# Kernel optimization log

Measured on AMD Instinct MI355X. Metric: run time of the kernel, lower is better.

Reference implementation:

```python
import jax, jax.numpy as jnp
import numpy as np

N_NODES = 50000
N_EDGES = 800000
IN_DIM = 2
HID = 256
OUT = 16
MLP_H = 256
N_MID = 10  # middle GCN layers (256->256); total 12 layers
EPS = 1e-5


def _bn(x, g, b):
    # BatchNorm1d forward with batch statistics (training-mode math, deterministic)
    m = jnp.mean(x, axis=0)
    v = jnp.var(x, axis=0)
    return (x - m) * jax.lax.rsqrt(v + EPS) * g + b


def _conv(h, W, b, row, col, ew):
    # CutGCNConv: linear transform then edge-weighted scatter-add (source->target)
    h = h @ W + b                      # [N, out]
    msg = ew[:, None] * h[row]         # gather + scale, [E, out]
    return jax.ops.segment_sum(msg, col, num_segments=N_NODES)


def setup_inputs() -> dict:
    key = jax.random.key(0)
    ks = iter(jax.random.split(key, 32))
    d = {}
    d["x"] = jax.random.normal(next(ks), (N_NODES, IN_DIM), dtype=jnp.float32)
    d["edge_index"] = jax.random.randint(next(ks), (2, N_EDGES), 0, N_NODES, dtype=jnp.int32)
    d["edge_weight"] = jax.random.uniform(next(ks), (N_EDGES,), dtype=jnp.float32)
    # GCN params
    d["W0"] = jax.random.normal(next(ks), (IN_DIM, HID), dtype=jnp.float32) / np.sqrt(IN_DIM)
    d["b0"] = jnp.zeros((HID,), jnp.float32)
    d["Wm"] = jax.random.normal(next(ks), (N_MID, HID, HID), dtype=jnp.float32) / np.sqrt(HID)
    d["bm"] = jnp.zeros((N_MID, HID), jnp.float32)
    d["Wl"] = jax.random.normal(next(ks), (HID, OUT), dtype=jnp.float32) / np.sqrt(HID)
    d["bl"] = jnp.zeros((OUT,), jnp.float32)
    # BatchNorms: one before each GCN layer + one after the stack
    d["bn0_g"] = jnp.ones((IN_DIM,), jnp.float32); d["bn0_b"] = jnp.zeros((IN_DIM,), jnp.float32)
    d["bnm_g"] = jnp.ones((N_MID + 1, HID), jnp.float32); d["bnm_b"] = jnp.zeros((N_MID + 1, HID), jnp.float32)
    d["bno_g"] = jnp.ones((OUT,), jnp.float32); d["bno_b"] = jnp.zeros((OUT,), jnp.float32)
    # edge MLP params
    d["mW1"] = jax.random.normal(next(ks), (2 * OUT, MLP_H), dtype=jnp.float32) / np.sqrt(2 * OUT)
    d["mb1"] = jnp.zeros((MLP_H,), jnp.float32)
    d["mbn_g"] = jnp.ones((MLP_H,), jnp.float32); d["mbn_b"] = jnp.zeros((MLP_H,), jnp.float32)
    d["mW2"] = jax.random.normal(next(ks), (MLP_H, 1), dtype=jnp.float32) / np.sqrt(MLP_H)
    d["mb2"] = jnp.zeros((1,), jnp.float32)
    return d


def reference(x, edge_index, edge_weight, W0, b0, Wm, bm, Wl, bl,
              bn0_g, bn0_b, bnm_g, bnm_b, bno_g, bno_b,
              mW1, mb1, mbn_g, mbn_b, mW2, mb2):
    row, col = edge_index[0], edge_index[1]
    # GCN stack (dropout is identity in eval; ReLU after each conv)
    h = jax.nn.relu(_conv(_bn(x, bn0_g, bn0_b), W0, b0, row, col, edge_weight))
    for i in range(N_MID):
        h = jax.nn.relu(_conv(_bn(h, bnm_g[i], bnm_b[i]), Wm[i], bm[i], row, col, edge_weight))
    h = jax.nn.relu(_conv(_bn(h, bnm_g[N_MID], bnm_b[N_MID]), Wl, bl, row, col, edge_weight))
    h = _bn(h, bno_g, bno_b)  # final BatchNorm on gnn_out_dims

    def mlp(e):  # e: [E, 2*OUT]
        z = jax.nn.relu(_bn(e @ mW1 + mb1, mbn_g, mbn_b))
        return (z @ mW2 + mb2)[:, 0]

    hr, hc = h[row], h[col]
    p1 = mlp(jnp.concatenate([hr, hc], axis=1))
    # roll(shifts=16, dims=1) on a 32-wide tensor swaps the halves
    p2 = mlp(jnp.concatenate([hc, hr], axis=1))
    return jax.nn.sigmoid(0.5 * (p1 + p2))
```

## Files before the change

### kernel.cpp

```cpp
#include <hip/hip_runtime.h>
#include <hip/hip_bf16.h>
#include <hip/hip_fp16.h>
#include <math.h>

#define NNODES 50000
#define NEDGES 800000

#define OFF_CW       0ull
#define OFF_DOUT     401408ull
#define OFF_STATS2   602112ull
#define OFF_SP8      606208ull
#define OFF_MOM      966656ull
#define ZERO_END     1017856ull
#define OFF_ST       1017856ull
#define OFF_ABW      1019904ull
#define OFF_WIN      1026048ull
#define OFF_OFFSETS  1226752ull
#define OFF_SROW     1427456ull
#define OFF_SEW      4627456ull
#define OFF_RANK     7827456ull
#define OFF_WT       11027456ull
#define OFF_WP       12338176ull
#define OFF_BUFQ     12371968ull
#define OFF_BUFP     37971968ull
#define ALI_TMP16    0ull
#define ALI_HRAW     3276800ull
#define ALI_Z        6553600ull
#define ALI_AGGZ     8388608ull

typedef __attribute__((ext_vector_type(8))) _Float16 f16x8;
typedef __attribute__((ext_vector_type(4))) float f32x4;

union H4 { ushort4 u; __half h[4]; };
union US8 { uint4 u; __half h[8]; };
union HU { ushort u; __half h; };

static __device__ inline ushort f2h(float f) {
    HU cv; cv.h = __float2half(f); return cv.u;
}
static __device__ inline float h2f(ushort u) {
    HU cv; cv.u = u; return __half2float(cv.h);
}


__global__ void hist_kernel(const int* __restrict__ ei, const float* __restrict__ ew,
                            unsigned long long* __restrict__ cw, int* __restrict__ dout,
                            int* __restrict__ rank, int E) {
    for (int i = blockIdx.x * blockDim.x + threadIdx.x; i < E; i += gridDim.x * blockDim.x) {
        int r = ei[i];
        int c = ei[E + i];
        unsigned long long pack = (1ull << 40) |
            (unsigned long long)__float2uint_rn(ew[i] * 1048576.f);
        unsigned long long old = atomicAdd(&cw[c], pack);
        rank[i] = (int)(old >> 40);
        atomicAdd(&dout[r], 1);
    }
}

__global__ void scan_kernel(const unsigned long long* __restrict__ cw,
                            int* __restrict__ offsets, float* __restrict__ w_in, int N) {
    __shared__ int wsum[16];
    __shared__ int carry_s;
    int tid = threadIdx.x;
    int lane = tid & 63, w = tid >> 6;
    if (tid == 0) carry_s = 0;
    __syncthreads();
    for (int base = 0; base < N; base += 1024) {
        int v = 0;
        if (base + tid < N) {
            unsigned long long cv = cw[base + tid];
            v = (int)(cv >> 40);
            w_in[base + tid] = (float)(cv & 0xFFFFFFFFFFull) * (1.f / 1048576.f);
        }
        int x = v;
#pragma unroll
        for (int off = 1; off < 64; off <<= 1) {
            int y = __shfl_up(x, off);
            if (lane >= off) x += y;
        }
        if (lane == 63) wsum[w] = x;
        __syncthreads();
        if (w == 0 && lane < 16) {
            int s = wsum[lane];
#pragma unroll
            for (int off = 1; off < 16; off <<= 1) {
                int y = __shfl_up(s, off);
                if (lane >= off) s += y;
            }
            wsum[lane] = s;
        }
        __syncthreads();
        int wbase = (w > 0) ? wsum[w - 1] : 0;
        int incl = carry_s + wbase + x;
        if (base + tid < N) offsets[base + tid] = incl - v;
        __syncthreads();
        if (tid == 0) carry_s += wsum[15];
        __syncthreads();
    }
    if (tid == 0) offsets[N] = carry_s;
}

__global__ void scatter_kernel(const int* __restrict__ ei, const float* __restrict__ ew,
                               const int* __restrict__ offsets, const int* __restrict__ rank,
                               int* __restrict__ srow, float* __restrict__ sew, int E) {
    for (int i = blockIdx.x * blockDim.x + threadIdx.x; i < E; i += gridDim.x * blockDim.x) {
        int c = ei[E + i];
        int p = offsets[c] + rank[i];
        srow[p] = ei[i];
        sew[p] = ew[i];
    }
}


__global__ __launch_bounds__(256) void wconv(const float* __restrict__ Wm,
                                             ushort* __restrict__ Wt) {
    __shared__ float tile[32][33];
    int b = blockIdx.x;
    int layer = b >> 6, t = b & 63;
    int tk = (t >> 3) << 5, tn = (t & 7) << 5;
    int tid = threadIdx.x;
    int r = tid >> 5, c = tid & 31;
    const float* W = Wm + layer * 65536;
#pragma unroll
    for (int i = 0; i < 4; i++) tile[r + i * 8][c] = W[(tk + r + i * 8) * 256 + tn + c];
    __syncthreads();
#pragma unroll
    for (int i = 0; i < 4; i++) {
        int n = tn + r + i * 8, k = tk + c;
        Wt[layer * 65536 + n * 256 + k] = f2h(tile[c][r + i * 8]);
    }
}

__global__ void wprep(const float* __restrict__ mW1, ushort* __restrict__ Wp) {
    int tid = threadIdx.x;
    for (int n = tid; n < 512; n += 256) {
        for (int k = 0; k < 32; k++) {
            float v;
            if (n < 256) v = mW1[k * 256 + n];
            else {
                int n2 = n - 256;
                v = (k < 16) ? mW1[(16 + k) * 256 + n2] : mW1[(k - 16) * 256 + n2];
            }
            Wp[n * 32 + k] = f2h(v);
        }
    }
}


__global__ __launch_bounds__(256) void colstats_wr(const float* __restrict__ h,
                                                   float* __restrict__ sums, int C, int M) {
    int gtid = blockIdx.x * blockDim.x + threadIdx.x;
    int lane = threadIdx.x & 63;
    int c = gtid % C;
    int r = gtid / C;
    int stride = (gridDim.x * blockDim.x) / C;
    float s = 0.f, q = 0.f;
    for (; r < M; r += stride) {
        float v = h[r * C + c];
        s += v; q += v * v;
    }
    for (int m = 32; m >= C; m >>= 1) {
        s += __shfl_xor(s, m);
        q += __shfl_xor(q, m);
    }
    if (lane < C) {
        atomicAdd(&sums[c], s);
        atomicAdd(&sums[C + c], q);
    }
}

__global__ void bn_finalize(const float* __restrict__ sums, const float* __restrict__ g,
                            const float* __restrict__ b, float* __restrict__ st, int C, int M) {
    int c = threadIdx.x;
    if (c >= C) return;
    float mean = sums[c] / (float)M;
    float var  = sums[C + c] / (float)M - mean * mean;
    float sc = g[c] * rsqrtf(var + 1e-5f);
    st[c] = sc;
    st[C + c] = b[c] - mean * sc;
}

__global__ void bn_finalize16(const float* __restrict__ sp, const float* __restrict__ g,
                              const float* __restrict__ b, float* __restrict__ st, int M) {
    int c = threadIdx.x;
    float s = 0.f, q = 0.f;
#pragma unroll
    for (int p = 0; p < 16; p++) { s += sp[p * 512 + c]; q += sp[p * 512 + 256 + c]; }
    float mean = s / (float)M;
    float var  = q / (float)M - mean * mean;
    float sc = g[c] * rsqrtf(var + 1e-5f);
    st[c] = sc;
    st[256 + c] = b[c] - mean * sc;
}


__global__ __launch_bounds__(256) void gemm_mfma(const __half* __restrict__ H,
                                                 const ushort* __restrict__ Wt,
                                                 const float* __restrict__ bias,
                                                 const float* __restrict__ sp,
                                                 const float* __restrict__ g,
                                                 const float* __restrict__ b,
                                                 __half* __restrict__ out, int M) {
    __shared__ __attribute__((aligned(16))) ushort Ah[128][40];
    __shared__ __attribute__((aligned(16))) ushort Bh[128][40];
    __shared__ __attribute__((aligned(16))) float st_s[512];
    int tid = threadIdx.x;
    int wid = tid >> 6, lane = tid & 63;
    int m0 = blockIdx.x * 128;
    int n0 = blockIdx.y * 128;
    const ushort* Hu = (const ushort*)H;

    {
        float s = 0.f, q = 0.f;
#pragma unroll
        for (int p = 0; p < 16; p++) { s += sp[p * 512 + tid]; q += sp[p * 512 + 256 + tid]; }
        float invM = 1.f / (float)M;
        float mean = s * invM;
        float var  = q * invM - mean * mean;
        float sc = g[tid] * rsqrtf(var + 1e-5f);
        st_s[tid] = sc;
        st_s[256 + tid] = b[tid] - mean * sc;
    }
    __syncthreads();

    f32x4 acc[2][8];
#pragma unroll
    for (int m = 0; m < 2; m++)
#pragma unroll
        for (int n = 0; n < 8; n++) acc[m][n] = (f32x4){0.f, 0.f, 0.f, 0.f};

    int sr = tid >> 3;
    int kq = (tid & 7) << 2;
    int fr = lane & 15;
    int qo = (lane >> 4) << 3;
    int mrow = wid << 5;

    for (int k0 = 0; k0 < 256; k0 += 32) {
#pragma unroll
        for (int t = 0; t < 4; t++) {
            int r = sr + t * 32;
            int gr = m0 + r; if (gr >= M) gr = M - 1;
            H4 h4; h4.u = *(const ushort4*)(Hu + gr * 256 + k0 + kq);
            float4 s4 = *(const float4*)(st_s + k0 + kq);
            float4 t4 = *(const float4*)(st_s + 256 + k0 + kq);
            ushort4 vh;
            vh.x = f2h(__half2float(h4.h[0]) * s4.x + t4.x);
            vh.y = f2h(__half2float(h4.h[1]) * s4.y + t4.y);
            vh.z = f2h(__half2float(h4.h[2]) * s4.z + t4.z);
            vh.w = f2h(__half2float(h4.h[3]) * s4.w + t4.w);
            *(ushort4*)&Ah[r][kq] = vh;
            ushort4 bh = *(const ushort4*)(Wt + (n0 + r) * 256 + k0 + kq);
            *(ushort4*)&Bh[r][kq] = bh;
        }
        __syncthreads();

        f16x8 a0 = *(const f16x8*)&Ah[mrow + fr][qo];
        f16x8 a1 = *(const f16x8*)&Ah[mrow + 16 + fr][qo];
#pragma unroll
        for (int nt = 0; nt < 8; nt++) {
            f16x8 bb = *(const f16x8*)&Bh[nt * 16 + fr][qo];
            acc[0][nt] = __builtin_amdgcn_mfma_f32_16x16x32_f16(a0, bb, acc[0][nt], 0, 0, 0);
            acc[1][nt] = __builtin_amdgcn_mfma_f32_16x16x32_f16(a1, bb, acc[1][nt], 0, 0, 0);
        }
        __syncthreads();
    }

#pragma unroll
    for (int mt = 0; mt < 2; mt++) {
        int gmb = m0 + mrow + mt * 16 + ((lane >> 4) << 2);
#pragma unroll
        for (int nt = 0; nt < 8; nt++) {
            int gn = n0 + nt * 16 + fr;
            float bv = bias[gn];
#pragma unroll
            for (int j = 0; j < 4; j++) {
                int gm = gmb + j;
                if (gm < M) out[gm * 256 + gn] = __float2half(acc[mt][nt][j] + bv);
            }
        }
    }
}


__global__ __launch_bounds__(256) void spmm_f16w(const __half* __restrict__ T,
                                                 const int* __restrict__ srow,
                                                 const float* __restrict__ sew,
                                                 const int* __restrict__ off,
                                                 __half* __restrict__ outp,
                                                 float* __restrict__ sp, int N) {
    __shared__ float red[4][512];
    int tid = threadIdx.x;
    int wid = tid >> 6, lane = tid & 63;
    int hh = lane >> 5;
    int li = lane & 31;
    int colb = li << 3;
    const ushort* Tu = (const ushort*)T;
    ushort* Ou = (ushort*)outp;
    float cs[8] = {0, 0, 0, 0, 0, 0, 0, 0}, cq[8] = {0, 0, 0, 0, 0, 0, 0, 0};
    int gw = blockIdx.x * 4 + wid, nw = gridDim.x * 4;
    for (int n = gw; n < N; n += nw) {
        int e0 = off[n], e1 = off[n + 1];
        float acc[8] = {0, 0, 0, 0, 0, 0, 0, 0};
        int e = e0;
        for (; e + 7 < e1; e += 8) {
            int rr[4]; float wv[4]; US8 v[4];
#pragma unroll
            for (int i = 0; i < 4; i++) { rr[i] = srow[e + 2 * i + hh]; wv[i] = sew[e + 2 * i + hh]; }
#pragma unroll
            for (int i = 0; i < 4; i++) v[i].u = *(const uint4*)(Tu + rr[i] * 256 + colb);
#pragma unroll
            for (int i = 0; i < 4; i++)
#pragma unroll
                for (int j = 0; j < 8; j++) acc[j] += wv[i] * __half2float(v[i].h[j]);
        }
        for (; e < e1; e += 2) {
            if (e + hh < e1) {
                int r = srow[e + hh]; float w = sew[e + hh];
                US8 v; v.u = *(const uint4*)(Tu + r * 256 + colb);
#pragma unroll
                for (int j = 0; j < 8; j++) acc[j] += w * __half2float(v.h[j]);
            }
        }
        US8 o;
#pragma unroll
        for (int j = 0; j < 8; j++) {
            float other = __shfl(acc[j], lane ^ 32, 64);
            float s = fmaxf(acc[j] + other, 0.f);
            o.h[j] = __float2half(s);
            if (hh == 0) { cs[j] += s; cq[j] += s * s; }
        }
        if (hh == 0) *(uint4*)(Ou + n * 256 + colb) = o.u;
    }
    if (hh == 0) {
#pragma unroll
        for (int j = 0; j < 8; j++) {
            red[wid][colb + j] = cs[j];
            red[wid][256 + colb + j] = cq[j];
        }
    }
    __syncthreads();
    float* dst = sp + (blockIdx.x & 15) * 512;
    for (int i = tid; i < 512; i += 256)
        atomicAdd(&dst[i], red[0][i] + red[1][i] + red[2][i] + red[3][i]);
}

__global__ __launch_bounds__(256) void spmm_small(const float* __restrict__ T,
                                                  const int* __restrict__ srow,
                                                  const float* __restrict__ sew,
                                                  const int* __restrict__ off,
                                                  float* __restrict__ out,
                                                  int C, int N, int relu) {
    int npb = blockDim.x / C;
    int local = threadIdx.x / C;
    int c = threadIdx.x % C;
    int n = blockIdx.x * npb + local;
    if (n >= N) return;
    int e0 = off[n], e1 = off[n + 1];
    float acc = 0.f;
    for (int e = e0; e < e1; ++e) acc += sew[e] * T[srow[e] * C + c];
    if (relu) acc = fmaxf(acc, 0.f);
    out[n * C + c] = acc;
}


__global__ __launch_bounds__(256) void layer0_fin(const float* __restrict__ agg2,
                                                  const float* __restrict__ w_in,
                                                  const float* __restrict__ st,
                                                  const float* __restrict__ W0,
                                                  const float* __restrict__ b0,
                                                  __half* __restrict__ h,
                                                  float* __restrict__ sp, int N) {
    int j = threadIdx.x;
    float w0j = W0[j], w1j = W0[256 + j], b0j = b0[j];
    float s0 = st[0], s1 = st[1], t0 = st[2], t1 = st[3];
    float cs = 0.f, cq = 0.f;
    for (int n = blockIdx.x; n < N; n += gridDim.x) {
        float wi = w_in[n];
        float a0 = agg2[n * 2 + 0] * s0 + wi * t0;
        float a1 = agg2[n * 2 + 1] * s1 + wi * t1;
        float v = fmaxf(a0 * w0j + a1 * w1j + wi * b0j, 0.f);
        h[n * 256 + j] = __float2half(v);
        cs += v; cq += v * v;
    }
    float* dst = sp + (blockIdx.x & 15) * 512;
    atomicAdd(&dst[j], cs);
    atomicAdd(&dst[256 + j], cq);
}


__global__ __launch_bounds__(256) void gemm16(const __half* __restrict__ H,
                                              const float* __restrict__ Wl,
                                              const float* __restrict__ bl,
                                              const float* __restrict__ st,
                                              float* __restrict__ out, int M) {
    __shared__ float Hs[16][256];
    __shared__ float Ws[256][16];
    int tid = threadIdx.x;
    int n0 = blockIdx.x << 4;
    const ushort* Hu = (const ushort*)H;
    for (int i = tid; i < 4096; i += 256) Ws[i >> 4][i & 15] = Wl[i];
    for (int i = tid; i < 4096; i += 256) {
        int r = i >> 8, k = i & 255;
        int n = n0 + r;
        float hv = 0.f;
        if (n < M) hv = h2f(Hu[n * 256 + k]) * st[k] + st[256 + k];
        Hs[r][k] = hv;
    }
    __syncthreads();
    int r = tid >> 4, j = tid & 15;
    float acc = bl[j];
    for (int k = 0; k < 256; k++) acc += Hs[r][k] * Ws[k][j];
    if (n0 + r < M) out[(n0 + r) * 16 + j] = acc;
}


__global__ void zprep(const float* __restrict__ hraw, const float* __restrict__ st,
                      ushort* __restrict__ Z, int NE) {
    int i = blockIdx.x * blockDim.x + threadIdx.x;
    if (i >= NE) return;
    int c = i & 15;
    Z[i] = f2h(hraw[i] * st[c] + st[16 + c]);
}


__global__ __launch_bounds__(256) void aggz_spmm(const ushort* __restrict__ Z,
                                                 const int* __restrict__ srow,
                                                 const int* __restrict__ off,
                                                 float* __restrict__ aggz, int N) {
    int local = threadIdx.x >> 4;
    int c = threadIdx.x & 15;
    int n = blockIdx.x * 16 + local;
    if (n >= N) return;
    int e0 = off[n], e1 = off[n + 1];
    float acc = 0.f;
    for (int e = e0; e < e1; ++e) acc += h2f(Z[srow[e] * 16 + c]);
    aggz[n * 16 + c] = acc;
}


__global__ __launch_bounds__(256) void zmom(const ushort* __restrict__ Z,
                                            const float* __restrict__ aggz,
                                            const int* __restrict__ dout,
                                            const unsigned long long* __restrict__ cw,
                                            float* __restrict__ MOM, int N) {
    __shared__ float zs[128][17];
    __shared__ float az[128][17];
    __shared__ float dw[128][2];
    int tid = threadIdx.x;
    int i = tid >> 4, j = tid & 15;
    float p = 0.f, r = 0.f, m = 0.f, sdo = 0.f, sdi = 0.f;
    for (int base = blockIdx.x * 128; base < N; base += gridDim.x * 128) {
        int cnt = N - base; if (cnt > 128) cnt = 128;
        for (int t = tid; t < 2048; t += 256) {
            int n = t >> 4, c = t & 15;
            if (n < cnt) {
                zs[n][c] = h2f(Z[(base + n) * 16 + c]);
                az[n][c] = aggz[(base + n) * 16 + c];
            } else { zs[n][c] = 0.f; az[n][c] = 0.f; }
        }
        for (int t = tid; t < 128; t += 256) {
            if (t < cnt) {
                dw[t][0] = (float)dout[base + t];
                dw[t][1] = (float)(int)(cw[base + t] >> 40);
            } else { dw[t][0] = 0.f; dw[t][1] = 0.f; }
        }
        __syncthreads();
        for (int n = 0; n < 128; n++) {
            float zi = zs[n][i], zj = zs[n][j];
            float d0 = dw[n][0], d1 = dw[n][1];
            float zz = zi * zj;
            p += d0 * zz;
            r += d1 * zz;
            m += az[n][i] * zj;
            if (i == 0) { sdo += d0 * zj; sdi += d1 * zj; }
        }
        __syncthreads();
    }
    float* dst = MOM + (blockIdx.x & 15) * 800;
    atomicAdd(&dst[tid], p);
    atomicAdd(&dst[256 + tid], r);
    atomicAdd(&dst[512 + tid], m);
    if (i == 0) { atomicAdd(&dst[768 + j], sdo); atomicAdd(&dst[784 + j], sdi); }
}


__global__ __launch_bounds__(256) void mlp_ab(const float* __restrict__ MOM,
                                              const float* __restrict__ mW1,
                                              const float* __restrict__ g,
                                              const float* __restrict__ b,
                                              const float* __restrict__ mW2,
                                              float* __restrict__ abw, int E) {
    __shared__ float P[256], R[256], Mm[256], Sdo[16], Sdi[16];
    int tid = threadIdx.x;
    float sp = 0.f, sr = 0.f, sm = 0.f;
#pragma unroll
    for (int q = 0; q < 16; q++) {
        sp += MOM[q * 800 + tid];
        sr += MOM[q * 800 + 256 + tid];
        sm += MOM[q * 800 + 512 + tid];
    }
    P[tid] = sp; R[tid] = sr; Mm[tid] = sm;
    if (tid < 16) {
        float a = 0.f, c = 0.f;
#pragma unroll
        for (int q = 0; q < 16; q++) { a += MOM[q * 800 + 768 + tid]; c += MOM[q * 800 + 784 + tid]; }
        Sdo[tid] = a; Sdi[tid] = c;
    }
    __syncthreads();
    int j = tid;
    float A[16], B[16];
#pragma unroll
    for (int k = 0; k < 16; k++) { A[k] = mW1[k * 256 + j]; B[k] = mW1[(16 + k) * 256 + j]; }
    float apa = 0.f, brb = 0.f, amb = 0.f, bpb = 0.f, ara = 0.f, bma = 0.f;
    float aso = 0.f, bso = 0.f, asi = 0.f, bsi = 0.f;
    for (int i2 = 0; i2 < 16; i2++) {
        float Ai = A[i2], Bi = B[i2];
        aso += Ai * Sdo[i2]; bso += Bi * Sdo[i2];
        asi += Ai * Sdi[i2]; bsi += Bi * Sdi[i2];
#pragma unroll
        for (int k = 0; k < 16; k++) {
            float Pik = P[i2 * 16 + k], Rik = R[i2 * 16 + k], Mik = Mm[i2 * 16 + k];
            apa += Ai * Pik * A[k]; brb += Bi * Rik * B[k]; amb += Ai * Mik * B[k];
            bpb += Bi * Pik * B[k]; ara += Ai * Rik * A[k]; bma += Bi * Mik * A[k];
        }
    }
    float invE = 1.f / (float)E;
    float mu1 = (aso + bsi) * invE;
    float mu2 = (bso + asi) * invE;
    float e21 = (apa + brb + 2.f * amb) * invE;
    float e22 = (bpb + ara + 2.f * bma) * invE;
    float v1 = e21 - mu1 * mu1;
    float v2 = e22 - mu2 * mu2;
    float a1 = g[j] * rsqrtf(v1 + 1e-5f);
    float a2 = g[j] * rsqrtf(v2 + 1e-5f);
    abw[j] = a1;                 abw[256 + j] = a2;
    abw[512 + j] = b[j] - mu1 * a1; abw[768 + j] = b[j] - mu2 * a2;
    abw[1024 + j] = mW2[j];      abw[1280 + j] = mW2[j];
}


__global__ __launch_bounds__(256) void edge_mfma(const ushort* __restrict__ Z,
                                                 const int* __restrict__ ei,
                                                 const ushort* __restrict__ Wp,
                                                 const float* __restrict__ abw,
                                                 const float* __restrict__ mb2,
                                                 float* __restrict__ out, int E) {
    __shared__ __attribute__((aligned(16))) ushort As[256][40];
    __shared__ __attribute__((aligned(16))) ushort Bs[512][40];
    int tid = threadIdx.x;
    int wid = tid >> 6, lane = tid & 63;
    int fr = lane & 15, qo = (lane >> 4) << 3;

    for (int i = tid * 4; i < 512 * 32; i += 1024) {
        int n = i >> 5, k = i & 31;
        *(ushort4*)&Bs[n][k] = *(const ushort4*)(Wp + i);
    }
    int e0 = blockIdx.x * 256;
    {
        int e = e0 + tid;
        int r = 0, c = 0;
        if (e < E) { r = ei[e]; c = ei[E + e]; }
        uint4 z0 = *(const uint4*)(Z + r * 16);
        uint4 z1 = *(const uint4*)(Z + r * 16 + 8);
        uint4 z2 = *(const uint4*)(Z + c * 16);
        uint4 z3 = *(const uint4*)(Z + c * 16 + 8);
        *(uint4*)&As[tid][0]  = z0; *(uint4*)&As[tid][8]  = z1;
        *(uint4*)&As[tid][16] = z2; *(uint4*)&As[tid][24] = z3;
    }
    __syncthreads();

    f16x8 a[4];
#pragma unroll
    for (int mt = 0; mt < 4; mt++) a[mt] = *(const f16x8*)&As[(wid * 4 + mt) * 16 + fr][qo];
    float pacc[4][4];
#pragma unroll
    for (int mt = 0; mt < 4; mt++)
#pragma unroll
        for (int j = 0; j < 4; j++) pacc[mt][j] = 0.f;
    float mb2v = mb2[0];

    for (int n = 0; n < 32; n++) {
        f16x8 bfr = *(const f16x8*)&Bs[n * 16 + fr][qo];
        int col = n * 16 + fr;
        float av = abw[col], bv = abw[512 + col], wv = abw[1024 + col];
#pragma unroll
        for (int mt = 0; mt < 4; mt++) {
            f32x4 c0 = {0.f, 0.f, 0.f, 0.f};
            c0 = __builtin_amdgcn_mfma_f32_16x16x32_f16(a[mt], bfr, c0, 0, 0, 0);
#pragma unroll
            for (int j = 0; j < 4; j++)
                pacc[mt][j] += fmaxf(c0[j] * av + bv, 0.f) * wv;
        }
    }

#pragma unroll
    for (int mt = 0; mt < 4; mt++)
#pragma unroll
        for (int j = 0; j < 4; j++) {
            float p = pacc[mt][j];
            p += __shfl_xor(p, 1);
            p += __shfl_xor(p, 2);
            p += __shfl_xor(p, 4);
            p += __shfl_xor(p, 8);
            if (fr == 0) {
                int row = (wid * 4 + mt) * 16 + ((lane >> 4) << 2) + j;
                int e = e0 + row;
                if (e < E) out[e] = 1.f / (1.f + expf(-(0.5f * p + mb2v)));
            }
        }
}


extern "C" void kernel_launch(void* const* d_in, const int* in_sizes, int n_in,
                              void* d_out, int out_size, void* d_ws, size_t ws_size,
                              hipStream_t stream) {
    const float* x     = (const float*)d_in[0];
    const int*   ei    = (const int*)d_in[1];
    const float* ew    = (const float*)d_in[2];
    const float* W0    = (const float*)d_in[3];
    const float* b0    = (const float*)d_in[4];
    const float* Wm    = (const float*)d_in[5];
    const float* bm    = (const float*)d_in[6];
    const float* Wl    = (const float*)d_in[7];
    const float* bl    = (const float*)d_in[8];
    const float* bn0_g = (const float*)d_in[9];
    const float* bn0_b = (const float*)d_in[10];
    const float* bnm_g = (const float*)d_in[11];
    const float* bnm_b = (const float*)d_in[12];
    const float* bno_g = (const float*)d_in[13];
    const float* bno_b = (const float*)d_in[14];
    const float* mW1   = (const float*)d_in[15];
    const float* mbn_g = (const float*)d_in[17];
    const float* mbn_b = (const float*)d_in[18];
    const float* mW2   = (const float*)d_in[19];
    const float* mb2   = (const float*)d_in[20];
    float* outp = (float*)d_out;

    char* ws = (char*)d_ws;
    unsigned long long* cw = (unsigned long long*)(ws + OFF_CW);
    int*    dout    = (int*)(ws + OFF_DOUT);
    float*  stats2  = (float*)(ws + OFF_STATS2);
    float*  sp8     = (float*)(ws + OFF_SP8);
    float*  MOM     = (float*)(ws + OFF_MOM);
    float*  st      = (float*)(ws + OFF_ST);
    float*  abw     = (float*)(ws + OFF_ABW);
    float*  w_in    = (float*)(ws + OFF_WIN);
    int*    offsets = (int*)(ws + OFF_OFFSETS);
    int*    srow    = (int*)(ws + OFF_SROW);
    float*  sew     = (float*)(ws + OFF_SEW);
    int*    rank    = (int*)(ws + OFF_RANK);
    ushort* Wt      = (ushort*)(ws + OFF_WT);
    ushort* Wp      = (ushort*)(ws + OFF_WP);
    __half* bufQ    = (__half*)(ws + OFF_BUFQ);
    __half* bufP    = (__half*)(ws + OFF_BUFP);
    float*  agg2    = (float*)(ws + OFF_BUFQ + ALI_TMP16);
    float*  tmp16   = (float*)(ws + OFF_BUFQ + ALI_TMP16);
    float*  hraw    = (float*)(ws + OFF_BUFQ + ALI_HRAW);
    ushort* Z       = (ushort*)(ws + OFF_BUFQ + ALI_Z);
    float*  aggz    = (float*)(ws + OFF_BUFQ + ALI_AGGZ);

    const int N = NNODES, E = NEDGES;

    hipMemsetAsync(ws, 0, ZERO_END, stream);

    hist_kernel<<<1024, 256, 0, stream>>>(ei, ew, cw, dout, rank, E);
    wconv<<<640, 256, 0, stream>>>(Wm, Wt);
    wprep<<<1, 256, 0, stream>>>(mW1, Wp);
    scan_kernel<<<1, 1024, 0, stream>>>(cw, offsets, w_in, N);
    scatter_kernel<<<1024, 256, 0, stream>>>(ei, ew, offsets, rank, srow, sew, E);

    colstats_wr<<<64, 256, 0, stream>>>(x, stats2 + 0 * 512, 2, N);
    bn_finalize<<<1, 256, 0, stream>>>(stats2 + 0 * 512, bn0_g, bn0_b, st, 2, N);
    spmm_small<<<(N + 127) / 128, 256, 0, stream>>>(x, srow, sew, offsets, agg2, 2, N, 0);
    layer0_fin<<<512, 256, 0, stream>>>(agg2, w_in, st, W0, b0, bufP, sp8 + 0 * 8192, N);

    for (int i = 0; i < 10; i++) {
        gemm_mfma<<<dim3((N + 127) / 128, 2), 256, 0, stream>>>(
            bufP, Wt + i * 65536, bm + i * 256,
            sp8 + i * 8192, bnm_g + i * 256, bnm_b + i * 256, bufQ, N);
        spmm_f16w<<<2048, 256, 0, stream>>>(bufQ, srow, sew, offsets, bufP,
                                            sp8 + (i + 1) * 8192, N);
    }

    bn_finalize16<<<1, 256, 0, stream>>>(sp8 + 10 * 8192, bnm_g + 10 * 256,
                                         bnm_b + 10 * 256, st, N);
    gemm16<<<(N + 15) / 16, 256, 0, stream>>>(bufP, Wl, bl, st, tmp16, N);
    spmm_small<<<(N + 15) / 16, 256, 0, stream>>>(tmp16, srow, sew, offsets, hraw, 16, N, 1);

    colstats_wr<<<64, 256, 0, stream>>>(hraw, stats2 + 1 * 512, 16, N);
    bn_finalize<<<1, 256, 0, stream>>>(stats2 + 1 * 512, bno_g, bno_b, st, 16, N);
    zprep<<<(N * 16 + 255) / 256, 256, 0, stream>>>(hraw, st, Z, N * 16);

    aggz_spmm<<<(N + 15) / 16, 256, 0, stream>>>(Z, srow, offsets, aggz, N);
    zmom<<<256, 256, 0, stream>>>(Z, aggz, dout, cw, MOM, N);
    mlp_ab<<<1, 256, 0, stream>>>(MOM, mW1, mbn_g, mbn_b, mW2, abw, E);

    edge_mfma<<<(E + 255) / 256, 256, 0, stream>>>(Z, ei, Wp, abw, mb2, outp, E);
}
```

Measured before the change: 1.544 ms.

## Fold BatchNorm into weights, pack CSR edges, rewrite edge MLP via abs identity

Folds each middle layer's BatchNorm scale and shift into a per-layer copy of the fp16 weights and bias, computed by a small bnw kernel. The GEMM A-tile load then becomes a plain copy instead of a per-element normalize. Row index and edge weight are packed into one int2 array, so each SpMM does one gather instead of two. The edge MLP folds the BN scale into Wp2 and rewrites relu(x) as (x+|x|)/2, so the linear half becomes a per-node dot product (gprep) and the kernel accumulates only |c+b|. This drops the shared-memory B staging, but the weights are no longer normalized in fp32 first, which may change rounding.

```diff
diff --git a/kernel.cpp b/kernel.cpp
--- a/kernel.cpp
+++ b/kernel.cpp
@@ -16,11 +16,12 @@
 #define OFF_ABW      1019904ull
 #define OFF_WIN      1026048ull
 #define OFF_OFFSETS  1226752ull
-#define OFF_SROW     1427456ull
-#define OFF_SEW      4627456ull
+#define OFF_SE       1427456ull
 #define OFF_RANK     7827456ull
+#define ALI_WT2      0ull
+#define ALI_BIAS2    131072ull
+#define ALI_G        132096ull
 #define OFF_WT       11027456ull
-#define OFF_WP       12338176ull
 #define OFF_BUFQ     12371968ull
 #define OFF_BUFP     37971968ull
 #define ALI_TMP16    0ull
@@ -102,12 +103,11 @@
 
 __global__ void scatter_kernel(const int* __restrict__ ei, const float* __restrict__ ew,
                                const int* __restrict__ offsets, const int* __restrict__ rank,
-                               int* __restrict__ srow, float* __restrict__ sew, int E) {
+                               int2* __restrict__ se, int E) {
     for (int i = blockIdx.x * blockDim.x + threadIdx.x; i < E; i += gridDim.x * blockDim.x) {
         int c = ei[E + i];
         int p = offsets[c] + rank[i];
-        srow[p] = ei[i];
-        sew[p] = ew[i];
+        se[p] = make_int2(ei[i], __float_as_int(ew[i]));
     }
 }
 
@@ -128,21 +128,6 @@
     for (int i = 0; i < 4; i++) {
         int n = tn + r + i * 8, k = tk + c;
         Wt[layer * 65536 + n * 256 + k] = f2h(tile[c][r + i * 8]);
-    }
-}
-
-__global__ void wprep(const float* __restrict__ mW1, ushort* __restrict__ Wp) {
-    int tid = threadIdx.x;
-    for (int n = tid; n < 512; n += 256) {
-        for (int k = 0; k < 32; k++) {
-            float v;
-            if (n < 256) v = mW1[k * 256 + n];
-            else {
-                int n2 = n - 256;
-                v = (k < 16) ? mW1[(16 + k) * 256 + n2] : mW1[(k - 16) * 256 + n2];
-            }
-            Wp[n * 32 + k] = f2h(v);
-        }
     }
 }
 
@@ -194,22 +179,15 @@
 }
 
 
-__global__ __launch_bounds__(256) void gemm_mfma(const __half* __restrict__ H,
-                                                 const ushort* __restrict__ Wt,
-                                                 const float* __restrict__ bias,
-                                                 const float* __restrict__ sp,
-                                                 const float* __restrict__ g,
-                                                 const float* __restrict__ b,
-                                                 __half* __restrict__ out, int M) {
-    __shared__ __attribute__((aligned(16))) ushort Ah[128][40];
-    __shared__ __attribute__((aligned(16))) ushort Bh[128][40];
-    __shared__ __attribute__((aligned(16))) float st_s[512];
-    int tid = threadIdx.x;
-    int wid = tid >> 6, lane = tid & 63;
-    int m0 = blockIdx.x * 128;
-    int n0 = blockIdx.y * 128;
-    const ushort* Hu = (const ushort*)H;
-
+__global__ __launch_bounds__(256) void bnw(const float* __restrict__ sp,
+                                           const float* __restrict__ g,
+                                           const float* __restrict__ b,
+                                           const ushort* __restrict__ Wt,
+                                           const float* __restrict__ bias,
+                                           ushort* __restrict__ Wt2,
+                                           float* __restrict__ bias2, int M) {
+    __shared__ float st_s[512];
+    int tid = threadIdx.x;
     {
         float s = 0.f, q = 0.f;
 #pragma unroll
@@ -222,6 +200,34 @@
         st_s[256 + tid] = b[tid] - mean * sc;
     }
     __syncthreads();
+    int n = blockIdx.x * 4 + (tid >> 6);
+    int k4 = (tid & 63) << 2;
+    ushort4 w4 = *(const ushort4*)(Wt + n * 256 + k4);
+    float4 s4 = *(const float4*)(st_s + k4);
+    float4 t4 = *(const float4*)(st_s + 256 + k4);
+    float w0 = h2f(w4.x), w1 = h2f(w4.y), w2 = h2f(w4.z), w3 = h2f(w4.w);
+    ushort4 o;
+    o.x = f2h(w0 * s4.x); o.y = f2h(w1 * s4.y);
+    o.z = f2h(w2 * s4.z); o.w = f2h(w3 * s4.w);
+    *(ushort4*)(Wt2 + n * 256 + k4) = o;
+    float part = w0 * t4.x + w1 * t4.y + w2 * t4.z + w3 * t4.w;
+#pragma unroll
+    for (int m = 1; m < 64; m <<= 1) part += __shfl_xor(part, m);
+    if ((tid & 63) == 0) bias2[n] = bias[n] + part;
+}
+
+
+__global__ __launch_bounds__(256) void gemm_mfma(const __half* __restrict__ H,
+                                                 const ushort* __restrict__ Wt2,
+                                                 const float* __restrict__ bias2,
+                                                 __half* __restrict__ out, int M) {
+    __shared__ __attribute__((aligned(16))) ushort Ah[128][40];
+    __shared__ __attribute__((aligned(16))) ushort Bh[128][40];
+    int tid = threadIdx.x;
+    int wid = tid >> 6, lane = tid & 63;
+    int m0 = blockIdx.x * 128;
+    int n0 = blockIdx.y * 128;
+    const ushort* Hu = (const ushort*)H;
 
     f32x4 acc[2][8];
 #pragma unroll
@@ -240,17 +246,8 @@
         for (int t = 0; t < 4; t++) {
             int r = sr + t * 32;
             int gr = m0 + r; if (gr >= M) gr = M - 1;
-            H4 h4; h4.u = *(const ushort4*)(Hu + gr * 256 + k0 + kq);
-            float4 s4 = *(const float4*)(st_s + k0 + kq);
-            float4 t4 = *(const float4*)(st_s + 256 + k0 + kq);
-            ushort4 vh;
-            vh.x = f2h(__half2float(h4.h[0]) * s4.x + t4.x);
-            vh.y = f2h(__half2float(h4.h[1]) * s4.y + t4.y);
-            vh.z = f2h(__half2float(h4.h[2]) * s4.z + t4.z);
-            vh.w = f2h(__half2float(h4.h[3]) * s4.w + t4.w);
-            *(ushort4*)&Ah[r][kq] = vh;
-            ushort4 bh = *(const ushort4*)(Wt + (n0 + r) * 256 + k0 + kq);
-            *(ushort4*)&Bh[r][kq] = bh;
+            *(ushort4*)&Ah[r][kq] = *(const ushort4*)(Hu + gr * 256 + k0 + kq);
+            *(ushort4*)&Bh[r][kq] = *(const ushort4*)(Wt2 + (n0 + r) * 256 + k0 + kq);
         }
         __syncthreads();
 
@@ -271,7 +268,7 @@
 #pragma unroll
         for (int nt = 0; nt < 8; nt++) {
             int gn = n0 + nt * 16 + fr;
-            float bv = bias[gn];
+            float bv = bias2[gn];
 #pragma unroll
             for (int j = 0; j < 4; j++) {
                 int gm = gmb + j;
@@ -283,8 +280,7 @@
 
 
 __global__ __launch_bounds__(256) void spmm_f16w(const __half* __restrict__ T,
-                                                 const int* __restrict__ srow,
-                                                 const float* __restrict__ sew,
+                                                 const int2* __restrict__ se,
                                                  const int* __restrict__ off,
                                                  __half* __restrict__ outp,
                                                  float* __restrict__ sp, int N) {
@@ -303,20 +299,23 @@
         float acc[8] = {0, 0, 0, 0, 0, 0, 0, 0};
         int e = e0;
         for (; e + 7 < e1; e += 8) {
-            int rr[4]; float wv[4]; US8 v[4];
-#pragma unroll
-            for (int i = 0; i < 4; i++) { rr[i] = srow[e + 2 * i + hh]; wv[i] = sew[e + 2 * i + hh]; }
-#pragma unroll
-            for (int i = 0; i < 4; i++) v[i].u = *(const uint4*)(Tu + rr[i] * 256 + colb);
-#pragma unroll
-            for (int i = 0; i < 4; i++)
-#pragma unroll
-                for (int j = 0; j < 8; j++) acc[j] += wv[i] * __half2float(v[i].h[j]);
+            int2 s[4]; US8 v[4];
+#pragma unroll
+            for (int i = 0; i < 4; i++) s[i] = se[e + 2 * i + hh];
+#pragma unroll
+            for (int i = 0; i < 4; i++) v[i].u = *(const uint4*)(Tu + s[i].x * 256 + colb);
+#pragma unroll
+            for (int i = 0; i < 4; i++) {
+                float w = __int_as_float(s[i].y);
+#pragma unroll
+                for (int j = 0; j < 8; j++) acc[j] += w * __half2float(v[i].h[j]);
+            }
         }
         for (; e < e1; e += 2) {
             if (e + hh < e1) {
-                int r = srow[e + hh]; float w = sew[e + hh];
-                US8 v; v.u = *(const uint4*)(Tu + r * 256 + colb);
+                int2 s = se[e + hh];
+                float w = __int_as_float(s.y);
+                US8 v; v.u = *(const uint4*)(Tu + s.x * 256 + colb);
 #pragma unroll
                 for (int j = 0; j < 8; j++) acc[j] += w * __half2float(v.h[j]);
             }
@@ -345,8 +344,7 @@
 }
 
 __global__ __launch_bounds__(256) void spmm_small(const float* __restrict__ T,
-                                                  const int* __restrict__ srow,
-                                                  const float* __restrict__ sew,
+                                                  const int2* __restrict__ se,
                                                   const int* __restrict__ off,
                                                   float* __restrict__ out,
                                                   int C, int N, int relu) {
@@ -357,7 +355,10 @@
     if (n >= N) return;
     int e0 = off[n], e1 = off[n + 1];
     float acc = 0.f;
-    for (int e = e0; e < e1; ++e) acc += sew[e] * T[srow[e] * C + c];
+    for (int e = e0; e < e1; ++e) {
+        int2 s = se[e];
+        acc += __int_as_float(s.y) * T[s.x * C + c];
+    }
     if (relu) acc = fmaxf(acc, 0.f);
     out[n * C + c] = acc;
 }
@@ -424,7 +425,7 @@
 
 
 __global__ __launch_bounds__(256) void aggz_spmm(const ushort* __restrict__ Z,
-                                                 const int* __restrict__ srow,
+                                                 const int2* __restrict__ se,
                                                  const int* __restrict__ off,
                                                  float* __restrict__ aggz, int N) {
     int local = threadIdx.x >> 4;
@@ -433,7 +434,7 @@
     if (n >= N) return;
     int e0 = off[n], e1 = off[n + 1];
     float acc = 0.f;
-    for (int e = e0; e < e1; ++e) acc += h2f(Z[srow[e] * 16 + c]);
+    for (int e = e0; e < e1; ++e) acc += h2f(Z[se[e].x * 16 + c]);
     aggz[n * 16 + c] = acc;
 }
 
@@ -489,9 +490,12 @@
                                               const float* __restrict__ g,
                                               const float* __restrict__ b,
                                               const float* __restrict__ mW2,
-                                              float* __restrict__ abw, int E) {
+                                              float* __restrict__ abw,
+                                              ushort* __restrict__ Wp2, int E) {
     __shared__ float P[256], R[256], Mm[256], Sdo[16], Sdi[16];
-    int tid = threadIdx.x;
+    __shared__ float gsh[33];
+    int tid = threadIdx.x;
+    if (tid < 33) gsh[tid] = 0.f;
     float sp = 0.f, sr = 0.f, sm = 0.f;
 #pragma unroll
     for (int q = 0; q < 16; q++) {
@@ -529,32 +533,67 @@
     float mu2 = (bso + asi) * invE;
     float e21 = (apa + brb + 2.f * amb) * invE;
     float e22 = (bpb + ara + 2.f * bma) * invE;
-    float v1 = e21 - mu1 * mu1;
-    float v2 = e22 - mu2 * mu2;
-    float a1 = g[j] * rsqrtf(v1 + 1e-5f);
-    float a2 = g[j] * rsqrtf(v2 + 1e-5f);
-    abw[j] = a1;                 abw[256 + j] = a2;
-    abw[512 + j] = b[j] - mu1 * a1; abw[768 + j] = b[j] - mu2 * a2;
-    abw[1024 + j] = mW2[j];      abw[1280 + j] = mW2[j];
+    float a1 = g[j] * rsqrtf(e21 - mu1 * mu1 + 1e-5f);
+    float a2 = g[j] * rsqrtf(e22 - mu2 * mu2 + 1e-5f);
+    float b1p = b[j] - mu1 * a1;
+    float b2p = b[j] - mu2 * a2;
+    float w = mW2[j];
+    abw[j] = b1p; abw[256 + j] = b2p;
+    abw[512 + j] = w; abw[768 + j] = w;
+#pragma unroll
+    for (int k = 0; k < 16; k++) {
+        Wp2[j * 32 + k]            = f2h(a1 * A[k]);
+        Wp2[j * 32 + 16 + k]       = f2h(a1 * B[k]);
+        Wp2[(256 + j) * 32 + k]    = f2h(a2 * B[k]);
+        Wp2[(256 + j) * 32 + 16 + k] = f2h(a2 * A[k]);
+    }
+#pragma unroll
+    for (int k = 0; k < 16; k++) {
+        atomicAdd(&gsh[k],      w * (a1 * A[k] + a2 * B[k]));
+        atomicAdd(&gsh[16 + k], w * (a1 * B[k] + a2 * A[k]));
+    }
+    atomicAdd(&gsh[32], w * (b1p + b2p));
+    __syncthreads();
+    if (tid < 32) abw[1024 + tid] = gsh[tid];
+    if (tid == 0) abw[1056] = gsh[32];
+}
+
+
+__global__ __launch_bounds__(256) void gprep(const ushort* __restrict__ Z,
+                                             const float* __restrict__ abw,
+                                             float2* __restrict__ G, int N) {
+    __shared__ float gs[32];
+    if (threadIdx.x < 32) gs[threadIdx.x] = abw[1024 + threadIdx.x];
+    __syncthreads();
+    int n = blockIdx.x * blockDim.x + threadIdx.x;
+    if (n >= N) return;
+    float g1 = 0.f, g2 = 0.f;
+#pragma unroll
+    for (int k = 0; k < 16; k++) {
+        float z = h2f(Z[n * 16 + k]);
+        g1 += z * gs[k];
+        g2 += z * gs[16 + k];
+    }
+    G[n] = make_float2(g1, g2);
 }
 
 
 __global__ __launch_bounds__(256) void edge_mfma(const ushort* __restrict__ Z,
                                                  const int* __restrict__ ei,
-                                                 const ushort* __restrict__ Wp,
+                                                 const ushort* __restrict__ Wp2,
                                                  const float* __restrict__ abw,
+                                                 const float2* __restrict__ G,
                                                  const float* __restrict__ mb2,
                                                  float* __restrict__ out, int E) {
     __shared__ __attribute__((aligned(16))) ushort As[256][40];
-    __shared__ __attribute__((aligned(16))) ushort Bs[512][40];
+    __shared__ float lin[256];
+    __shared__ float bbs[512], wws[512];
     int tid = threadIdx.x;
     int wid = tid >> 6, lane = tid & 63;
     int fr = lane & 15, qo = (lane >> 4) << 3;
 
-    for (int i = tid * 4; i < 512 * 32; i += 1024) {
-        int n = i >> 5, k = i & 31;
-        *(ushort4*)&Bs[n][k] = *(const ushort4*)(Wp + i);
-    }
+    for (int i = tid; i < 512; i += 256) { bbs[i] = abw[i]; wws[i] = abw[512 + i]; }
+    float cb = abw[1056];
     int e0 = blockIdx.x * 256;
     {
         int e = e0 + tid;
@@ -566,6 +605,8 @@
         uint4 z3 = *(const uint4*)(Z + c * 16 + 8);
         *(uint4*)&As[tid][0]  = z0; *(uint4*)&As[tid][8]  = z1;
         *(uint4*)&As[tid][16] = z2; *(uint4*)&As[tid][24] = z3;
+        float2 gr = G[r], gc = G[c];
+        lin[tid] = gr.x + gc.y + cb;
     }
     __syncthreads();
 
@@ -580,16 +621,16 @@
     float mb2v = mb2[0];
 
     for (int n = 0; n < 32; n++) {
-        f16x8 bfr = *(const f16x8*)&Bs[n * 16 + fr][qo];
+        f16x8 bfr = *(const f16x8*)(Wp2 + (n * 16 + fr) * 32 + qo);
         int col = n * 16 + fr;
-        float av = abw[col], bv = abw[512 + col], wv = abw[1024 + col];
+        float bv = bbs[col], wv = wws[col];
 #pragma unroll
         for (int mt = 0; mt < 4; mt++) {
             f32x4 c0 = {0.f, 0.f, 0.f, 0.f};
             c0 = __builtin_amdgcn_mfma_f32_16x16x32_f16(a[mt], bfr, c0, 0, 0, 0);
 #pragma unroll
             for (int j = 0; j < 4; j++)
-                pacc[mt][j] += fmaxf(c0[j] * av + bv, 0.f) * wv;
+                pacc[mt][j] += wv * fabsf(c0[j] + bv);
         }
     }
 
@@ -605,7 +646,7 @@
             if (fr == 0) {
                 int row = (wid * 4 + mt) * 16 + ((lane >> 4) << 2) + j;
                 int e = e0 + row;
-                if (e < E) out[e] = 1.f / (1.f + expf(-(0.5f * p + mb2v)));
+                if (e < E) out[e] = 1.f / (1.f + expf(-(0.25f * (lin[row] + p) + mb2v)));
             }
         }
 }
@@ -646,18 +687,20 @@
     float*  abw     = (float*)(ws + OFF_ABW);
     float*  w_in    = (float*)(ws + OFF_WIN);
     int*    offsets = (int*)(ws + OFF_OFFSETS);
-    int*    srow    = (int*)(ws + OFF_SROW);
-    float*  sew     = (float*)(ws + OFF_SEW);
+    int2*   se      = (int2*)(ws + OFF_SE);
     int*    rank    = (int*)(ws + OFF_RANK);
     ushort* Wt      = (ushort*)(ws + OFF_WT);
-    ushort* Wp      = (ushort*)(ws + OFF_WP);
     __half* bufQ    = (__half*)(ws + OFF_BUFQ);
     __half* bufP    = (__half*)(ws + OFF_BUFP);
+    ushort* Wt2     = (ushort*)(ws + OFF_RANK + ALI_WT2);
+    float*  bias2   = (float*)(ws + OFF_RANK + ALI_BIAS2);
+    float2* G       = (float2*)(ws + OFF_RANK + ALI_G);
     float*  agg2    = (float*)(ws + OFF_BUFQ + ALI_TMP16);
     float*  tmp16   = (float*)(ws + OFF_BUFQ + ALI_TMP16);
     float*  hraw    = (float*)(ws + OFF_BUFQ + ALI_HRAW);
     ushort* Z       = (ushort*)(ws + OFF_BUFQ + ALI_Z);
     float*  aggz    = (float*)(ws + OFF_BUFQ + ALI_AGGZ);
+    ushort* Wp2     = (ushort*)(ws + OFF_RANK + ALI_WT2);
 
     const int N = NNODES, E = NEDGES;
 
@@ -665,35 +708,35 @@
 
     hist_kernel<<<1024, 256, 0, stream>>>(ei, ew, cw, dout, rank, E);
     wconv<<<640, 256, 0, stream>>>(Wm, Wt);
-    wprep<<<1, 256, 0, stream>>>(mW1, Wp);
     scan_kernel<<<1, 1024, 0, stream>>>(cw, offsets, w_in, N);
-    scatter_kernel<<<1024, 256, 0, stream>>>(ei, ew, offsets, rank, srow, sew, E);
+    scatter_kernel<<<1024, 256, 0, stream>>>(ei, ew, offsets, rank, se, E);
 
     colstats_wr<<<64, 256, 0, stream>>>(x, stats2 + 0 * 512, 2, N);
     bn_finalize<<<1, 256, 0, stream>>>(stats2 + 0 * 512, bn0_g, bn0_b, st, 2, N);
-    spmm_small<<<(N + 127) / 128, 256, 0, stream>>>(x, srow, sew, offsets, agg2, 2, N, 0);
+    spmm_small<<<(N + 127) / 128, 256, 0, stream>>>(x, se, offsets, agg2, 2, N, 0);
     layer0_fin<<<512, 256, 0, stream>>>(agg2, w_in, st, W0, b0, bufP, sp8 + 0 * 8192, N);
 
     for (int i = 0; i < 10; i++) {
-        gemm_mfma<<<dim3((N + 127) / 128, 2), 256, 0, stream>>>(
-            bufP, Wt + i * 65536, bm + i * 256,
-            sp8 + i * 8192, bnm_g + i * 256, bnm_b + i * 256, bufQ, N);
-        spmm_f16w<<<2048, 256, 0, stream>>>(bufQ, srow, sew, offsets, bufP,
+        bnw<<<64, 256, 0, stream>>>(sp8 + i * 8192, bnm_g + i * 256, bnm_b + i * 256,
+                                    Wt + i * 65536, bm + i * 256, Wt2, bias2, N);
+        gemm_mfma<<<dim3((N + 127) / 128, 2), 256, 0, stream>>>(bufP, Wt2, bias2, bufQ, N);
+        spmm_f16w<<<2048, 256, 0, stream>>>(bufQ, se, offsets, bufP,
                                             sp8 + (i + 1) * 8192, N);
     }
 
     bn_finalize16<<<1, 256, 0, stream>>>(sp8 + 10 * 8192, bnm_g + 10 * 256,
                                          bnm_b + 10 * 256, st, N);
     gemm16<<<(N + 15) / 16, 256, 0, stream>>>(bufP, Wl, bl, st, tmp16, N);
-    spmm_small<<<(N + 15) / 16, 256, 0, stream>>>(tmp16, srow, sew, offsets, hraw, 16, N, 1);
+    spmm_small<<<(N + 15) / 16, 256, 0, stream>>>(tmp16, se, offsets, hraw, 16, N, 1);
 
     colstats_wr<<<64, 256, 0, stream>>>(hraw, stats2 + 1 * 512, 16, N);
     bn_finalize<<<1, 256, 0, stream>>>(stats2 + 1 * 512, bno_g, bno_b, st, 16, N);
     zprep<<<(N * 16 + 255) / 256, 256, 0, stream>>>(hraw, st, Z, N * 16);
 
-    aggz_spmm<<<(N + 15) / 16, 256, 0, stream>>>(Z, srow, offsets, aggz, N);
+    aggz_spmm<<<(N + 15) / 16, 256, 0, stream>>>(Z, se, offsets, aggz, N);
     zmom<<<256, 256, 0, stream>>>(Z, aggz, dout, cw, MOM, N);
-    mlp_ab<<<1, 256, 0, stream>>>(MOM, mW1, mbn_g, mbn_b, mW2, abw, E);
-
-    edge_mfma<<<(E + 255) / 256, 256, 0, stream>>>(Z, ei, Wp, abw, mb2, outp, E);
-}
+    mlp_ab<<<1, 256, 0, stream>>>(MOM, mW1, mbn_g, mbn_b, mW2, abw, Wp2, E);
+    gprep<<<(N + 255) / 256, 256, 0, stream>>>(Z, abw, G, N);
+
+    edge_mfma<<<(E + 255) / 256, 256, 0, stream>>>(Z, ei, Wp2, abw, G, mb2, outp, E);
+}
```

After: 1.724 ms. +11.6%, slower.
